# Optimization experiments

Measured on AMD Instinct MI355X. Metric: run time of the kernel, lower is better.

Reference implementation:

```python
import jax, jax.numpy as jnp
import numpy as np

N_NODES = 100_000
N_EDGES = 3_200_000
N_GRAPHS = 256
F_IN = 128


def setup_inputs() -> dict:
    key = jax.random.key(0)
    ks = jax.random.split(key, 12)
    x = jax.random.normal(ks[0], (N_NODES, F_IN), dtype=jnp.float32)
    edge_weight = jax.random.uniform(ks[1], (N_EDGES,), dtype=jnp.float32)
    W1 = jax.random.normal(ks[2], (F_IN, 16), dtype=jnp.float32) * (1.0 / np.sqrt(F_IN))
    b1 = jnp.zeros((16,), jnp.float32)
    W2 = jax.random.normal(ks[3], (16, 16), dtype=jnp.float32) * 0.25
    b2 = jnp.zeros((16,), jnp.float32)
    Wd2 = jax.random.normal(ks[4], (16, 16), dtype=jnp.float32) * 0.25
    bd2 = jnp.zeros((16,), jnp.float32)
    Wd3 = jax.random.normal(ks[5], (16, 2), dtype=jnp.float32) * 0.25
    bd3 = jnp.zeros((2,), jnp.float32)
    row = jax.random.randint(ks[6], (N_EDGES,), 0, N_NODES, dtype=jnp.int32)
    col = jax.random.randint(ks[7], (N_EDGES,), 0, N_NODES, dtype=jnp.int32)
    seg = jnp.sort(jax.random.randint(ks[8], (N_NODES,), 0, N_GRAPHS, dtype=jnp.int32))
    return {"x": x, "edge_weight": edge_weight, "W1": W1, "b1": b1, "W2": W2,
            "b2": b2, "Wd2": Wd2, "bd2": bd2, "Wd3": Wd3, "bd3": bd3,
            "row": row, "col": col, "seg": seg}


def _gcn_conv(x, row, col, w, kernel, bias):
    # Spektral GCNConv: out = A_norm @ (x @ kernel) + bias
    h = x @ kernel                                   # [N, C]
    msg = h[col] * w[:, None]                        # gather + weight, [E, C]
    agg = jax.ops.segment_sum(msg, row, num_segments=N_NODES)  # scatter-add
    return agg + bias


def reference(x, edge_weight, W1, b1, W2, b2, Wd2, bd2, Wd3, bd3, row, col, seg):
    h = jax.nn.elu(_gcn_conv(x, row, col, edge_weight, W1, b1))
    h = jax.nn.elu(_gcn_conv(h, row, col, edge_weight, W2, b2))
    pooled = jax.ops.segment_sum(h, seg, num_segments=N_GRAPHS)  # [G, 16]
    out = jax.nn.relu(pooled @ Wd2 + bd2)
    # Dropout is identity at inference time
    out = jax.nn.sigmoid(out @ Wd3 + bd3)            # [G, 2]
    return out
```

## Files before the change

### kernel.cpp

```cpp
#include <hip/hip_runtime.h>

#define N_NODES 100000
#define N_EDGES 3200000
#define N_GRAPHS 256

__global__ __launch_bounds__(256) void gemm1_kernel(const float* __restrict__ x,
                                                    const float* __restrict__ W1,
                                                    float* __restrict__ outA,
                                                    float* __restrict__ zeroB) {
    __shared__ float w1s[128 * 16];
    const int tid = threadIdx.x;
    {
        const float4* ws = (const float4*)W1;
        float4* wd = (float4*)w1s;
        wd[tid] = ws[tid];
        wd[tid + 256] = ws[tid + 256];
    }
    __syncthreads();
    const int node = blockIdx.x * 256 + tid;
    if (node >= N_NODES) return;
    const float4* xr = (const float4*)(x + (size_t)node * 128);
    float acc[16];
#pragma unroll
    for (int j = 0; j < 16; ++j) acc[j] = 0.f;
#pragma unroll 8
    for (int k4 = 0; k4 < 32; ++k4) {
        const float4 xv = xr[k4];
        const float* wr = &w1s[k4 * 64];
#pragma unroll
        for (int j = 0; j < 16; ++j)
            acc[j] = fmaf(xv.x, wr[j],
                     fmaf(xv.y, wr[16 + j],
                     fmaf(xv.z, wr[32 + j],
                     fmaf(xv.w, wr[48 + j], acc[j]))));
    }
    float4* dst = (float4*)(outA + (size_t)node * 16);
#pragma unroll
    for (int q = 0; q < 4; ++q)
        dst[q] = make_float4(acc[q * 4], acc[q * 4 + 1], acc[q * 4 + 2], acc[q * 4 + 3]);
    float4* bz = (float4*)(zeroB + (size_t)node * 16);
    const float4 z = make_float4(0.f, 0.f, 0.f, 0.f);
#pragma unroll
    for (int q = 0; q < 4; ++q) bz[q] = z;
}

__global__ __launch_bounds__(256) void gemm16f_kernel(float* __restrict__ Braw,
                                                      const float* __restrict__ bias,
                                                      const float* __restrict__ W,
                                                      float* __restrict__ outA) {
    __shared__ float wsm[256];
    __shared__ float bs[16];
    const int tid = threadIdx.x;
    wsm[tid] = W[tid];
    if (tid < 16) bs[tid] = bias[tid];
    __syncthreads();
    const int node = blockIdx.x * 256 + tid;
    if (node >= N_NODES) return;
    float4* hr = (float4*)(Braw + (size_t)node * 16);
    float hv[16];
#pragma unroll
    for (int q = 0; q < 4; ++q) {
        const float4 v = hr[q];
        float a0 = v.x + bs[q * 4 + 0], a1 = v.y + bs[q * 4 + 1];
        float a2 = v.z + bs[q * 4 + 2], a3 = v.w + bs[q * 4 + 3];
        hv[q * 4 + 0] = a0 > 0.f ? a0 : expm1f(a0);
        hv[q * 4 + 1] = a1 > 0.f ? a1 : expm1f(a1);
        hv[q * 4 + 2] = a2 > 0.f ? a2 : expm1f(a2);
        hv[q * 4 + 3] = a3 > 0.f ? a3 : expm1f(a3);
    }
    float acc[16];
#pragma unroll
    for (int j = 0; j < 16; ++j) acc[j] = 0.f;
#pragma unroll
    for (int k = 0; k < 16; ++k) {
#pragma unroll
        for (int j = 0; j < 16; ++j)
            acc[j] = fmaf(hv[k], wsm[k * 16 + j], acc[j]);
    }
    float4* dst = (float4*)(outA + (size_t)node * 16);
#pragma unroll
    for (int q = 0; q < 4; ++q)
        dst[q] = make_float4(acc[q * 4], acc[q * 4 + 1], acc[q * 4 + 2], acc[q * 4 + 3]);
    const float4 z = make_float4(0.f, 0.f, 0.f, 0.f);
#pragma unroll
    for (int q = 0; q < 4; ++q) hr[q] = z;
}

__global__ __launch_bounds__(256) void scatter_kernel(const float* __restrict__ h,
                                                      const float* __restrict__ w,
                                                      const int* __restrict__ row,
                                                      const int* __restrict__ col,
                                                      float* __restrict__ agg) {
    const long long t = (long long)blockIdx.x * 256 + threadIdx.x;
    const int e = (int)(t >> 4);
    const int ch = (int)(t & 15);
    const int r = row[e], c = col[e];
    const float wt = w[e];
    atomicAdd(agg + (size_t)r * 16 + ch, h[(size_t)c * 16 + ch] * wt);
}

__global__ __launch_bounds__(256) void poolg_kernel(const float* __restrict__ Braw,
                                                    const float* __restrict__ bias,
                                                    const int* __restrict__ seg,
                                                    float* __restrict__ pooled) {
    __shared__ float bs[16];
    __shared__ float red[256];
    const int g = blockIdx.x;
    const int tid = threadIdx.x;
    const int ch = tid & 15, grp = tid >> 4;
    if (tid < 16) bs[tid] = bias[tid];
    __syncthreads();
    int lo = 0, hi = N_NODES;
    while (lo < hi) { const int mid = (lo + hi) >> 1; if (seg[mid] < g) lo = mid + 1; else hi = mid; }
    const int start = lo;
    hi = N_NODES;
    while (lo < hi) { const int mid = (lo + hi) >> 1; if (seg[mid] < g + 1) lo = mid + 1; else hi = mid; }
    const int end = lo;
    float acc = 0.f;
    for (int n = start + grp; n < end; n += 16) {
        const float v = Braw[(size_t)n * 16 + ch] + bs[ch];
        acc += v > 0.f ? v : expm1f(v);
    }
    red[grp * 16 + ch] = acc;
    __syncthreads();
    if (tid < 16) {
        float s = 0.f;
#pragma unroll
        for (int q = 0; q < 16; ++q) s += red[q * 16 + tid];
        pooled[g * 16 + tid] = s;
    }
}

__global__ __launch_bounds__(256) void head_kernel(const float* __restrict__ pooled,
                                                   const float* __restrict__ Wd2,
                                                   const float* __restrict__ bd2,
                                                   const float* __restrict__ Wd3,
                                                   const float* __restrict__ bd3,
                                                   float* __restrict__ out) {
    __shared__ float w2[256], w3[32], b2s[16], b3s[2];
    const int tid = threadIdx.x;
    w2[tid] = Wd2[tid];
    if (tid < 32) w3[tid] = Wd3[tid];
    if (tid < 16) b2s[tid] = bd2[tid];
    if (tid < 2) b3s[tid] = bd3[tid];
    __syncthreads();
    const int g = tid;
    float p[16];
#pragma unroll
    for (int k = 0; k < 16; ++k) p[k] = pooled[g * 16 + k];
    float t[16];
#pragma unroll
    for (int j = 0; j < 16; ++j) {
        float acc = b2s[j];
#pragma unroll
        for (int k = 0; k < 16; ++k) acc = fmaf(p[k], w2[k * 16 + j], acc);
        t[j] = acc > 0.f ? acc : 0.f;
    }
#pragma unroll
    for (int m = 0; m < 2; ++m) {
        float acc = b3s[m];
#pragma unroll
        for (int j = 0; j < 16; ++j) acc = fmaf(t[j], w3[j * 2 + m], acc);
        out[g * 2 + m] = 1.f / (1.f + expf(-acc));
    }
}

extern "C" void kernel_launch(void* const* d_in, const int* in_sizes, int n_in,
                              void* d_out, int out_size, void* d_ws, size_t ws_size,
                              hipStream_t stream) {
    const float* x   = (const float*)d_in[0];
    const float* ew  = (const float*)d_in[1];
    const float* W1  = (const float*)d_in[2];
    const float* b1  = (const float*)d_in[3];
    const float* W2  = (const float*)d_in[4];
    const float* b2  = (const float*)d_in[5];
    const float* Wd2 = (const float*)d_in[6];
    const float* bd2 = (const float*)d_in[7];
    const float* Wd3 = (const float*)d_in[8];
    const float* bd3 = (const float*)d_in[9];
    const int* row   = (const int*)d_in[10];
    const int* col   = (const int*)d_in[11];
    const int* seg   = (const int*)d_in[12];
    float* out = (float*)d_out;

    float* A = (float*)d_ws;
    float* B = A + (size_t)N_NODES * 16;
    float* pooled = B + (size_t)N_NODES * 16;

    const int scatter_blocks = (int)(((long long)N_EDGES * 16) / 256);
    const int node_blocks = (N_NODES + 255) / 256;

    gemm1_kernel<<<node_blocks, 256, 0, stream>>>(x, W1, A, B);
    scatter_kernel<<<scatter_blocks, 256, 0, stream>>>(A, ew, row, col, B);

    gemm16f_kernel<<<node_blocks, 256, 0, stream>>>(B, b1, W2, A);
    scatter_kernel<<<scatter_blocks, 256, 0, stream>>>(A, ew, row, col, B);

    poolg_kernel<<<N_GRAPHS, 256, 0, stream>>>(B, b2, seg, pooled);
    head_kernel<<<1, 256, 0, stream>>>(pooled, Wd2, bd2, Wd3, bd3, out);
}
```

Measured before the change: 496.6 us.

## Split gemm1 K across thread pairs, precompute graph bounds, fuse pooling with head

The first projection now uses two threads per node. Each thread handles half of the 128 input features, and the partial sums are combined with a lane shuffle, giving more parallelism and shorter per-thread loops. The second GEMM kernel also writes per-graph node boundaries from the sorted segment array, which removes the binary searches in the pooling kernel. Pooling is unrolled four-wide and fused with the dense head, which drops one kernel launch and the pooled buffer. The fused head relies on intra-wavefront ordering of shared-memory writes with no barrier, which is fragile. The scatter kernels, which dominate the run time, are unchanged.

```diff
diff --git a/kernel.cpp b/kernel.cpp
--- a/kernel.cpp
+++ b/kernel.cpp
@@ -17,37 +17,61 @@
         wd[tid + 256] = ws[tid + 256];
     }
     __syncthreads();
-    const int node = blockIdx.x * 256 + tid;
+    const int gtid = blockIdx.x * 256 + tid;
+    const int node = gtid >> 1;
+    const int half = gtid & 1;
     if (node >= N_NODES) return;
-    const float4* xr = (const float4*)(x + (size_t)node * 128);
+    const float4* xr = (const float4*)(x + (size_t)node * 128 + half * 64);
     float acc[16];
 #pragma unroll
     for (int j = 0; j < 16; ++j) acc[j] = 0.f;
-#pragma unroll 8
-    for (int k4 = 0; k4 < 32; ++k4) {
+#pragma unroll 4
+    for (int k4 = 0; k4 < 16; ++k4) {
         const float4 xv = xr[k4];
-        const float* wr = &w1s[k4 * 64];
-#pragma unroll
-        for (int j = 0; j < 16; ++j)
-            acc[j] = fmaf(xv.x, wr[j],
-                     fmaf(xv.y, wr[16 + j],
-                     fmaf(xv.z, wr[32 + j],
-                     fmaf(xv.w, wr[48 + j], acc[j]))));
-    }
-    float4* dst = (float4*)(outA + (size_t)node * 16);
-#pragma unroll
-    for (int q = 0; q < 4; ++q)
-        dst[q] = make_float4(acc[q * 4], acc[q * 4 + 1], acc[q * 4 + 2], acc[q * 4 + 3]);
-    float4* bz = (float4*)(zeroB + (size_t)node * 16);
+        const float4* wk = (const float4*)&w1s[(half * 64 + k4 * 4) * 16];
+#pragma unroll
+        for (int kk = 0; kk < 4; ++kk) {
+            const float xs_ = (&xv.x)[kk];
+            const float4 wa = wk[kk * 4 + 0];
+            const float4 wb = wk[kk * 4 + 1];
+            const float4 wc = wk[kk * 4 + 2];
+            const float4 wdv = wk[kk * 4 + 3];
+            acc[0]  = fmaf(xs_, wa.x, acc[0]);
+            acc[1]  = fmaf(xs_, wa.y, acc[1]);
+            acc[2]  = fmaf(xs_, wa.z, acc[2]);
+            acc[3]  = fmaf(xs_, wa.w, acc[3]);
+            acc[4]  = fmaf(xs_, wb.x, acc[4]);
+            acc[5]  = fmaf(xs_, wb.y, acc[5]);
+            acc[6]  = fmaf(xs_, wb.z, acc[6]);
+            acc[7]  = fmaf(xs_, wb.w, acc[7]);
+            acc[8]  = fmaf(xs_, wc.x, acc[8]);
+            acc[9]  = fmaf(xs_, wc.y, acc[9]);
+            acc[10] = fmaf(xs_, wc.z, acc[10]);
+            acc[11] = fmaf(xs_, wc.w, acc[11]);
+            acc[12] = fmaf(xs_, wdv.x, acc[12]);
+            acc[13] = fmaf(xs_, wdv.y, acc[13]);
+            acc[14] = fmaf(xs_, wdv.z, acc[14]);
+            acc[15] = fmaf(xs_, wdv.w, acc[15]);
+        }
+    }
+#pragma unroll
+    for (int j = 0; j < 16; ++j) acc[j] += __shfl_xor(acc[j], 1);
+    const int co = half * 8;
+    float4* dst = (float4*)(outA + (size_t)node * 16 + co);
+    dst[0] = make_float4(acc[co + 0], acc[co + 1], acc[co + 2], acc[co + 3]);
+    dst[1] = make_float4(acc[co + 4], acc[co + 5], acc[co + 6], acc[co + 7]);
+    float4* bz = (float4*)(zeroB + (size_t)node * 16 + co);
     const float4 z = make_float4(0.f, 0.f, 0.f, 0.f);
-#pragma unroll
-    for (int q = 0; q < 4; ++q) bz[q] = z;
+    bz[0] = z;
+    bz[1] = z;
 }
 
 __global__ __launch_bounds__(256) void gemm16f_kernel(float* __restrict__ Braw,
                                                       const float* __restrict__ bias,
                                                       const float* __restrict__ W,
-                                                      float* __restrict__ outA) {
+                                                      float* __restrict__ outA,
+                                                      const int* __restrict__ seg,
+                                                      int* __restrict__ bnd) {
     __shared__ float wsm[256];
     __shared__ float bs[16];
     const int tid = threadIdx.x;
@@ -56,6 +80,13 @@
     __syncthreads();
     const int node = blockIdx.x * 256 + tid;
     if (node >= N_NODES) return;
+    {
+        const int sc = seg[node];
+        const int sp = (node == 0) ? -1 : seg[node - 1];
+        for (int g = sp + 1; g <= sc; ++g) bnd[g] = node;
+        if (node == N_NODES - 1)
+            for (int g = sc + 1; g <= N_GRAPHS; ++g) bnd[g] = N_NODES;
+    }
     float4* hr = (float4*)(Braw + (size_t)node * 16);
     float hv[16];
 #pragma unroll
@@ -99,69 +130,57 @@
     atomicAdd(agg + (size_t)r * 16 + ch, h[(size_t)c * 16 + ch] * wt);
 }
 
-__global__ __launch_bounds__(256) void poolg_kernel(const float* __restrict__ Braw,
-                                                    const float* __restrict__ bias,
-                                                    const int* __restrict__ seg,
-                                                    float* __restrict__ pooled) {
+__global__ __launch_bounds__(256) void poolgh_kernel(const float* __restrict__ Braw,
+                                                     const float* __restrict__ bias,
+                                                     const int* __restrict__ bnd,
+                                                     const float* __restrict__ Wd2,
+                                                     const float* __restrict__ bd2,
+                                                     const float* __restrict__ Wd3,
+                                                     const float* __restrict__ bd3,
+                                                     float* __restrict__ out) {
     __shared__ float bs[16];
     __shared__ float red[256];
+    __shared__ float ps[16];
+    __shared__ float ts[16];
     const int g = blockIdx.x;
     const int tid = threadIdx.x;
     const int ch = tid & 15, grp = tid >> 4;
     if (tid < 16) bs[tid] = bias[tid];
     __syncthreads();
-    int lo = 0, hi = N_NODES;
-    while (lo < hi) { const int mid = (lo + hi) >> 1; if (seg[mid] < g) lo = mid + 1; else hi = mid; }
-    const int start = lo;
-    hi = N_NODES;
-    while (lo < hi) { const int mid = (lo + hi) >> 1; if (seg[mid] < g + 1) lo = mid + 1; else hi = mid; }
-    const int end = lo;
+    const int start = bnd[g], end = bnd[g + 1];
     float acc = 0.f;
-    for (int n = start + grp; n < end; n += 16) {
+    int n = start + grp;
+    for (; n + 48 < end; n += 64) {
+        const float v0 = Braw[(size_t)n * 16 + ch] + bs[ch];
+        const float v1 = Braw[(size_t)(n + 16) * 16 + ch] + bs[ch];
+        const float v2 = Braw[(size_t)(n + 32) * 16 + ch] + bs[ch];
+        const float v3 = Braw[(size_t)(n + 48) * 16 + ch] + bs[ch];
+        acc += (v0 > 0.f ? v0 : expm1f(v0)) + (v1 > 0.f ? v1 : expm1f(v1))
+             + (v2 > 0.f ? v2 : expm1f(v2)) + (v3 > 0.f ? v3 : expm1f(v3));
+    }
+    for (; n < end; n += 16) {
         const float v = Braw[(size_t)n * 16 + ch] + bs[ch];
         acc += v > 0.f ? v : expm1f(v);
     }
-    red[grp * 16 + ch] = acc;
+    red[tid] = acc;
     __syncthreads();
     if (tid < 16) {
         float s = 0.f;
 #pragma unroll
         for (int q = 0; q < 16; ++q) s += red[q * 16 + tid];
-        pooled[g * 16 + tid] = s;
-    }
-}
-
-__global__ __launch_bounds__(256) void head_kernel(const float* __restrict__ pooled,
-                                                   const float* __restrict__ Wd2,
-                                                   const float* __restrict__ bd2,
-                                                   const float* __restrict__ Wd3,
-                                                   const float* __restrict__ bd3,
-                                                   float* __restrict__ out) {
-    __shared__ float w2[256], w3[32], b2s[16], b3s[2];
-    const int tid = threadIdx.x;
-    w2[tid] = Wd2[tid];
-    if (tid < 32) w3[tid] = Wd3[tid];
-    if (tid < 16) b2s[tid] = bd2[tid];
-    if (tid < 2) b3s[tid] = bd3[tid];
-    __syncthreads();
-    const int g = tid;
-    float p[16];
-#pragma unroll
-    for (int k = 0; k < 16; ++k) p[k] = pooled[g * 16 + k];
-    float t[16];
-#pragma unroll
-    for (int j = 0; j < 16; ++j) {
-        float acc = b2s[j];
-#pragma unroll
-        for (int k = 0; k < 16; ++k) acc = fmaf(p[k], w2[k * 16 + j], acc);
-        t[j] = acc > 0.f ? acc : 0.f;
-    }
-#pragma unroll
-    for (int m = 0; m < 2; ++m) {
-        float acc = b3s[m];
-#pragma unroll
-        for (int j = 0; j < 16; ++j) acc = fmaf(t[j], w3[j * 2 + m], acc);
-        out[g * 2 + m] = 1.f / (1.f + expf(-acc));
+        ps[tid] = s;
+        const int j = tid;
+        float a = bd2[j];
+#pragma unroll
+        for (int k = 0; k < 16; ++k) a = fmaf(ps[k], Wd2[k * 16 + j], a);
+        ts[j] = a > 0.f ? a : 0.f;
+        if (tid < 2) {
+            const int m = tid;
+            float o = bd3[m];
+#pragma unroll
+            for (int jj = 0; jj < 16; ++jj) o = fmaf(ts[jj], Wd3[jj * 2 + m], o);
+            out[g * 2 + m] = 1.f / (1.f + expf(-o));
+        }
     }
 }
 
@@ -185,17 +204,17 @@
 
     float* A = (float*)d_ws;
     float* B = A + (size_t)N_NODES * 16;
-    float* pooled = B + (size_t)N_NODES * 16;
+    int* bnd = (int*)(B + (size_t)N_NODES * 16);
 
     const int scatter_blocks = (int)(((long long)N_EDGES * 16) / 256);
+    const int g1_blocks = (N_NODES * 2 + 255) / 256;
     const int node_blocks = (N_NODES + 255) / 256;
 
-    gemm1_kernel<<<node_blocks, 256, 0, stream>>>(x, W1, A, B);
+    gemm1_kernel<<<g1_blocks, 256, 0, stream>>>(x, W1, A, B);
     scatter_kernel<<<scatter_blocks, 256, 0, stream>>>(A, ew, row, col, B);
 
-    gemm16f_kernel<<<node_blocks, 256, 0, stream>>>(B, b1, W2, A);
+    gemm16f_kernel<<<node_blocks, 256, 0, stream>>>(B, b1, W2, A, seg, bnd);
     scatter_kernel<<<scatter_blocks, 256, 0, stream>>>(A, ew, row, col, B);
 
-    poolg_kernel<<<N_GRAPHS, 256, 0, stream>>>(B, b2, seg, pooled);
-    head_kernel<<<1, 256, 0, stream>>>(pooled, Wd2, bd2, Wd3, bd3, out);
-}
+    poolgh_kernel<<<N_GRAPHS, 256, 0, stream>>>(B, b2, bnd, Wd2, bd2, Wd3, bd3, out);
+}
```

New measurement: 496.3 us. No clear change (-0.1%).
